# Performance work log

Hardware: AMD Instinct MI355X
Metric: run time of the kernel (lower is better)

The kernel has to match this reference:

```python
import jax, jax.numpy as jnp
import numpy as np

R_SPHERE = 3.0   # bounding_sphere_radius
NEAR = 0.0       # near_distance
FAR = 100.0      # far_distance
SECANT_STEPS = 4 # manifold_secant_steps
EPS = 1e-4
R0 = 1.0         # base radius of analytic manifold field


def setup_inputs() -> dict:
    key = jax.random.key(0)
    ks = jax.random.split(key, 6)
    B, R, L, H = 4, 8192, 4, 64
    rays_o = jax.random.normal(ks[0], (B, R, 3), dtype=jnp.float32) * 0.2  # origins inside sphere
    rd = jax.random.normal(ks[1], (B, R, 3), dtype=jnp.float32)
    rays_d = rd / jnp.linalg.norm(rd, axis=-1, keepdims=True)
    levels = jnp.linspace(0.5, -0.5, L, dtype=jnp.float32)  # manifold_levels parameter
    W1 = jax.random.normal(ks[2], (3, H), dtype=jnp.float32) * 0.3
    b1 = jnp.zeros((H,), dtype=jnp.float32)
    W2 = jax.random.normal(ks[3], (H, 1), dtype=jnp.float32) * 0.1
    b2 = jnp.zeros((1,), dtype=jnp.float32)
    rays_idx = jax.random.randint(ks[4], (B, R), 0, B, dtype=jnp.int64) if jax.config.jax_enable_x64 else jax.random.randint(ks[4], (B, R), 0, B, dtype=jnp.int32)
    mask_gt = jnp.ones((B, R), dtype=bool)
    return {"rays_o": rays_o, "rays_d": rays_d, "levels": levels, "W1": W1, "b1": b1,
            "W2": W2, "b2": b2, "mask_gt": mask_gt, "rays_idx": rays_idx, "num_samples": 64}


def _ray_march(rays_o, rays_d, levels, W1, b1, W2, b2, num_samples):
    B, Rn = rays_o.shape[:2]
    N = B * Rn
    L = levels.shape[0]
    o = rays_o.reshape(N, 3)
    d = rays_d.reshape(N, 3)

    def manifold_fn(x):
        # analytic stand-in for M(x_d, idx): scalar field + validity mask
        h = jnp.tanh(x @ W1 + b1)
        nrm = jnp.linalg.norm(x, axis=-1)
        s = (h @ W2)[..., 0] + b2[0] + (R0 - nrm)
        return s, nrm < R_SPHERE

    # ray-sphere intersection (unit-norm directions assumed, as in source)
    b = jnp.sum(o * d, axis=-1)
    c = jnp.sum(o * o, axis=-1) - R_SPHERE ** 2
    disc = b * b - c
    hit = disc > 0
    sq = jnp.sqrt(jnp.where(hit, disc, 1.0))
    d_near = jnp.maximum(-b - sq, NEAR)
    d_far = jnp.minimum(-b + sq, FAR)
    mask_bound = hit & (d_near < d_far)

    # stratified (uniform) depth samples, (N, S)
    t = jnp.linspace(0.0, 1.0, num_samples, dtype=rays_o.dtype)[None, :]
    ds = d_near[:, None] * (1 - t) + d_far[:, None] * t
    x_d = o[:, None, :] + d[:, None, :] * ds[..., None]  # (N, S, 3)
    scal, m_valid = manifold_fn(x_d)                      # (N, S)

    # --- find_closest_interval ---
    S = num_samples
    dep_f, dep_b = ds[:, :-1], ds[:, 1:]
    sc_f, sc_b = scal[:, :-1], scal[:, 1:]
    m_pair = m_valid[:, :-1] & m_valid[:, 1:]
    l3 = levels[None, :, None]                            # (1, L, 1)
    in_interval = (sc_f[:, None, :] >= l3) & (l3 >= sc_b[:, None, :]) & m_pair[:, None, :]
    rank = jnp.sign(l3 - sc_b[:, None, :]) * jnp.arange(S - 1, 0, -1, dtype=scal.dtype)
    ind_closest = jnp.argmax(rank, axis=2)                # (N, L)
    ind_lowest = jnp.broadcast_to(jnp.argmin(sc_b, axis=1)[:, None], (N, L))
    mask_surface = jnp.any(in_interval, axis=2)
    idx = jnp.where(mask_surface, ind_closest, ind_lowest)
    d_front = jnp.take_along_axis(dep_f, idx, axis=1)
    d_back = jnp.take_along_axis(dep_b, idx, axis=1)
    s_front = jnp.take_along_axis(sc_f, idx, axis=1)
    s_back = jnp.take_along_axis(sc_b, idx, axis=1)

    # --- find_exact_intersection ---
    lr = levels[None, :]                                  # (1, L)
    s_diff = s_front - s_back
    m_vdiff = jnp.abs(s_diff) > EPS
    mask_intersect = (s_front >= lr) & (lr >= s_back)
    mask_secant = mask_intersect & m_vdiff
    s_diff_safe = jnp.where(m_vdiff, s_diff, 1.0)
    d_secant = ((lr - s_back) * d_front + (s_front - lr) * d_back) / s_diff_safe
    d_init = jnp.where(mask_secant, d_secant, d_back)

    # secant refinement (fixed step count; masked full-array updates replace
    # torch's boolean-indexed subset updates with identical math on masked lanes)
    dfs, dbs, sfs, sbs, dcur = d_front, d_back, s_front, s_back, d_init
    for _ in range(SECANT_STEPS):
        x_mid = o[:, None, :] + dcur[..., None] * d[:, None, :]  # (N, L, 3)
        s_mid, mv = manifold_fn(x_mid)
        upf = (s_mid > lr) & mv
        upb = (s_mid < lr) & mv
        dfs = jnp.where(upf, dcur, dfs)
        sfs = jnp.where(upf, s_mid, sfs)
        dbs = jnp.where(upb, dcur, dbs)
        sbs = jnp.where(upb, s_mid, sbs)
        sd = sfs - sbs
        ok = jnp.abs(sd) > EPS
        dcur = jnp.where(ok, ((lr - sbs) * dfs + (sfs - lr) * dbs) / jnp.where(ok, sd, 1.0), dcur)
    d_intersect = jnp.where(mask_secant, dcur, d_init)

    # sort intersections by depth (use_presort=False branch)
    order = jnp.argsort(d_intersect, axis=1)
    d_intersect = jnp.take_along_axis(d_intersect, order, axis=1)
    mask_intersect = jnp.take_along_axis(mask_intersect, order, axis=1)

    dist = jnp.where(mask_bound[:, None], d_intersect, 0.0).reshape(B, Rn, L)
    mask = (mask_intersect & mask_bound[:, None]).reshape(B, Rn, L)
    return dist, mask


def reference(rays_o, rays_d, levels, W1, b1, W2, b2, mask_gt, rays_idx, num_samples):
    # mask_gt / rays_idx are unused in eval mode (use_gt_mask_when_training=False,
    # analytic manifold_fn ignores batch index), kept for signature fidelity.
    return _ray_march(rays_o, rays_d, levels, W1, b1, W2, b2, num_samples)
```

## Files before the change

kernel.cpp:

```cpp
#include <hip/hip_runtime.h>
#include <cstdint>

#define R_SPHEREf 3.0f
#define NEARf 0.0f
#define FARf 100.0f
#define SECANT_STEPS 4
#define EPSf 1e-4f
#define R0f 1.0f
#define Hh 64
#define Lc 4
#define Sn 64

#define C_HI 2.88539004325866699f
#define C_LO 3.8519227871e-08f

typedef unsigned long long u64;

__device__ __forceinline__ float fastdiv(float a, float b) {
    float rcp = __builtin_amdgcn_rcpf(b);
    rcp = __builtin_fmaf(rcp, __builtin_fmaf(-b, rcp, 1.0f), rcp);
    return a * rcp;
}

__global__ __launch_bounds__(256) void manifold_render_kernel(
    const float* __restrict__ rays_o, const float* __restrict__ rays_d,
    const float* __restrict__ levels, const float* __restrict__ W1,
    const float* __restrict__ b1, const float* __restrict__ W2,
    const float* __restrict__ b2, float* __restrict__ out, int N)
{
    __shared__ float4 abq[4][2][Hh];

    const int tid = threadIdx.x;
    const int wave = tid >> 6;
    const int lane = tid & 63;
    const int half = lane >> 5;
    const int sl5  = lane & 31;
    const int rbase = blockIdx.x * 8 + wave * 2;
    if (rbase >= N) return;
    const int r  = rbase + half;
    const int rr = (r < N) ? r : (N - 1);

    const float b2v = b2[0];
    float lvl[Lc];
#pragma unroll
    for (int j = 0; j < Lc; ++j) lvl[j] = levels[j];

    const float ox = rays_o[3 * rr], oy = rays_o[3 * rr + 1], oz = rays_o[3 * rr + 2];
    const float dx = rays_d[3 * rr], dy = rays_d[3 * rr + 1], dz = rays_d[3 * rr + 2];

    const float bq = ox * dx + oy * dy + oz * dz;
    const float cq = ox * ox + oy * oy + oz * oz - R_SPHEREf * R_SPHEREf;
    const float disc = bq * bq - cq;
    const bool hit = disc > 0.0f;
    const float sqv = __builtin_amdgcn_sqrtf(hit ? disc : 1.0f);
    const float d_near = fmaxf(-bq - sqv, NEARf);
    const float d_far  = fminf(-bq + sqv, FARf);
    const bool mask_bound = hit && (d_near < d_far);
    const float delta = (d_far - d_near) * (1.0f / 63.0f);

    const float w1x = W1[lane], w1y = W1[Hh + lane], w1z = W1[2 * Hh + lane];
    const float w2lane = W2[lane];
    const float zq = -2.0f * w2lane;
    const float zs = copysignf(fmaxf(fabsf(zq), 1e-30f), zq);
    const float rz = __builtin_amdgcn_rcpf(zs);
    {
        const float Ah = __builtin_fmaf(oz, w1z, __builtin_fmaf(oy, w1y,
                         __builtin_fmaf(ox, w1x, b1[lane])));
        const float Bh = __builtin_fmaf(dz, w1z, __builtin_fmaf(dy, w1y, dx * w1x));
        const float A2 = __builtin_fmaf(Ah, C_LO, Ah * C_HI);
        const float B2 = __builtin_fmaf(Bh, C_LO, Bh * C_HI);
        const float Gh = __builtin_amdgcn_exp2f(B2 * (8.0f * delta));
        abq[wave][half][lane] = make_float4(A2, B2, rz, Gh);
        const float oxo = __shfl_xor(ox, 32), oyo = __shfl_xor(oy, 32), ozo = __shfl_xor(oz, 32);
        const float dxo = __shfl_xor(dx, 32), dyo = __shfl_xor(dy, 32), dzo = __shfl_xor(dz, 32);
        const float dlo = __shfl_xor(delta, 32);
        const float Aho = __builtin_fmaf(ozo, w1z, __builtin_fmaf(oyo, w1y,
                          __builtin_fmaf(oxo, w1x, b1[lane])));
        const float Bho = __builtin_fmaf(dzo, w1z, __builtin_fmaf(dyo, w1y, dxo * w1x));
        const float A2o = __builtin_fmaf(Aho, C_LO, Aho * C_HI);
        const float B2o = __builtin_fmaf(Bho, C_LO, Bho * C_HI);
        const float Gho = __builtin_amdgcn_exp2f(B2o * (8.0f * dlo));
        abq[wave][half ^ 1][lane] = make_float4(A2o, B2o, rz, Gho);
    }

    float w2sum = w2lane;
#pragma unroll
    for (int m = 1; m < 64; m <<= 1) w2sum += __shfl_xor(w2sum, m);
    const float sbase = w2sum + b2v + R0f;

    const int hg2 = (lane >> 3) & 3;
    const int sl  = lane & 7;
    const float dsl = __builtin_fmaf((float)sl, delta, d_near);

    const float4* __restrict__ ab = &abq[wave][half][0];
    float v[16], G[16], K[16];
#pragma unroll
    for (int j = 0; j < 16; ++j) {
        const float4 q = ab[hg2 + 4 * j];
        const float y = __builtin_fmaf(dsl, q.y, q.x);
        const float e0 = __builtin_amdgcn_exp2f(y);
        v[j] = __builtin_fmaf(e0, q.z, q.z);
        G[j] = q.w;
        K[j] = __builtin_fmaf(-q.z, q.w, q.z);
    }

    float accA = 0.0f, accB = 0.0f;
#pragma unroll
    for (int it = 0; it < 8; ++it) {
        if (it > 0) {
#pragma unroll
            for (int j = 0; j < 16; ++j) v[j] = __builtin_fmaf(v[j], G[j], K[j]);
        }
        float part;
        {
            float tq[4];
#pragma unroll
            for (int qd = 0; qd < 4; ++qd) {
                const float a = v[4 * qd], b = v[4 * qd + 1];
                const float c = v[4 * qd + 2], d = v[4 * qd + 3];
                const float n01 = a + b, d01 = a * b;
                const float n23 = c + d, d23 = c * d;
                const float num = __builtin_fmaf(n23, d01, n01 * d23);
                const float den = d01 * d23;
                tq[qd] = num * __builtin_amdgcn_rcpf(den);
            }
            part = (tq[0] + tq[1]) + (tq[2] + tq[3]);
        }
        part += __shfl_xor(part, 8);
        part += __shfl_xor(part, 16);
        if (it == hg2)     accA = part;
        if (it == hg2 + 4) accB = part;
    }

    const float tA = (float)sl5 * (1.0f / 63.0f);
    const float dsvA = d_near * (1.0f - tA) + d_far * tA;
    const float tB = (float)(sl5 + 32) * (1.0f / 63.0f);
    const float dsvB = d_near * (1.0f - tB) + d_far * tB;
    const float xA0 = ox + dx * dsvA, xA1 = oy + dy * dsvA, xA2 = oz + dz * dsvA;
    const float xB0 = ox + dx * dsvB, xB1 = oy + dy * dsvB, xB2 = oz + dz * dsvB;
    const float nrmA = __builtin_amdgcn_sqrtf(xA0 * xA0 + xA1 * xA1 + xA2 * xA2);
    const float nrmB = __builtin_amdgcn_sqrtf(xB0 * xB0 + xB1 * xB1 + xB2 * xB2);
    const float scalA = (accA + sbase) - nrmA;
    const float scalB = (accB + sbase) - nrmB;
    const bool validA = nrmA < R_SPHEREf;
    const bool validB = nrmB < R_SPHEREf;

    const u64 LO32 = 0xFFFFFFFFull;
    const u64 mInt = 0x7FFFFFFFFFFFFFFFull;
#define ASSEMBLE(bA, bB) (half ? (((bA) >> 32) | ((bB) & ~LO32)) \
                               : (((bA) & LO32) | ((bB) << 32)))
    const u64 bVA = __ballot(validA), bVB = __ballot(validB);
    const u64 mV  = ASSEMBLE(bVA, bVB);
    const u64 mIB = mV & (mV >> 1) & mInt;

    float scbA = __shfl_down(scalA, 1);
    const float sB0 = __shfl(scalB, half << 5);
    if (sl5 == 31) scbA = sB0;
    const float scbB = __shfl_down(scalB, 1);
    const float keyA = scbA;
    const float keyB = (sl5 < 31) ? scbB : INFINITY;
    float mnv = fminf(keyA, keyB);
#pragma unroll
    for (int m = 1; m < 32; m <<= 1) mnv = fminf(mnv, __shfl_xor(mnv, m));
    const u64 eqA = __ballot(keyA == mnv), eqB = __ballot(keyB == mnv);
    const int ind_lowest = __builtin_ctzll(ASSEMBLE(eqA, eqB));

    bool mintb[Lc], msec[Lc];
    float dinit[Lc];
    float g_dfs = 0.f, g_dbs = 0.f, g_sfs = 0.f, g_sbs = 0.f, g_dcur = 0.f, g_lr = 0.f;
    const int gl = (lane >> 3) & 3;

#pragma unroll
    for (int lv = 0; lv < Lc; ++lv) {
        const float l = lvl[lv];
        const u64 bLA = __ballot(scalA < l),  bLB = __ballot(scalB < l);
        const u64 bEA = __ballot(scalA == l), bEB = __ballot(scalB == l);
        const u64 bL = ASSEMBLE(bLA, bLB);
        const u64 bE = ASSEMBLE(bEA, bEB);
        const u64 bP = (bL >> 1) & mInt;
        const u64 bZ = (bE >> 1) & mInt;
        const u64 bI = (~bL) & (bP | bZ) & mIB;
        const int ind_closest = bP ? __builtin_ctzll(bP)
                                   : (bZ ? __builtin_ctzll(bZ) : (Sn - 2));
        const int idx  = bI ? ind_closest : ind_lowest;
        const int idx1 = idx + 1;

        const int src0 = (half << 5) | (idx & 31);
        const float sfA = __shfl(scalA, src0), sfB = __shfl(scalB, src0);
        const float s_front = (idx < 32) ? sfA : sfB;
        const int src1 = (half << 5) | (idx1 & 31);
        const float sbA2 = __shfl(scalA, src1), sbB2 = __shfl(scalB, src1);
        const float s_back = (idx1 < 32) ? sbA2 : sbB2;

        const float tf = (float)idx  * (1.0f / 63.0f);
        const float d_front = d_near * (1.0f - tf) + d_far * tf;
        const float tb = (float)idx1 * (1.0f / 63.0f);
        const float d_back  = d_near * (1.0f - tb) + d_far * tb;

        const bool mi = (s_front >= l) && (l >= s_back);
        const float sd = s_front - s_back;
        const bool vd = fabsf(sd) > EPSf;
        const bool ms = mi && vd;
        const float d_sec = fastdiv((l - s_back) * d_front + (s_front - l) * d_back,
                                    vd ? sd : 1.0f);
        const float di = ms ? d_sec : d_back;

        mintb[lv] = mi; msec[lv] = ms; dinit[lv] = di;
        if (gl == lv) {
            g_dfs = d_front; g_dbs = d_back; g_sfs = s_front; g_sbs = s_back;
            g_dcur = di; g_lr = l;
        }
    }

    const int sub = lane & 7;
    const float4* __restrict__ ab2 = &abq[wave][half][0];
    float4 sq[8];
#pragma unroll
    for (int j = 0; j < 8; ++j) sq[j] = ab2[sub + 8 * j];

#pragma unroll
    for (int it = 0; it < SECANT_STEPS; ++it) {
        const float mx0 = ox + g_dcur * dx, mx1 = oy + g_dcur * dy, mx2 = oz + g_dcur * dz;
        const float mn = __builtin_amdgcn_sqrtf(mx0 * mx0 + mx1 * mx1 + mx2 * mx2);
        float vv[8];
#pragma unroll
        for (int j = 0; j < 8; ++j) {
            const float y = __builtin_fmaf(g_dcur, sq[j].y, sq[j].x);
            const float e = __builtin_amdgcn_exp2f(y);
            vv[j] = __builtin_fmaf(e, sq[j].z, sq[j].z);
        }
        float tp[4];
#pragma unroll
        for (int p = 0; p < 4; ++p) {
            const float n = vv[2 * p] + vv[2 * p + 1];
            const float d = vv[2 * p] * vv[2 * p + 1];
            tp[p] = n * __builtin_amdgcn_rcpf(d);
        }
        float part = (tp[0] + tp[1]) + (tp[2] + tp[3]);
        part += __shfl_xor(part, 1);
        part += __shfl_xor(part, 2);
        part += __shfl_xor(part, 4);
        const float s_mid = (part + sbase) - mn;
        const bool mv = mn < R_SPHEREf;
        const bool upf = (s_mid > g_lr) && mv;
        const bool upb = (s_mid < g_lr) && mv;
        if (upf) { g_dfs = g_dcur; g_sfs = s_mid; }
        if (upb) { g_dbs = g_dcur; g_sbs = s_mid; }
        const float sd2 = g_sfs - g_sbs;
        const bool ok = fabsf(sd2) > EPSf;
        if (ok) g_dcur = fastdiv((g_lr - g_sbs) * g_dfs + (g_sfs - g_lr) * g_dbs, sd2);
    }

    float v0g, v1g, v2g, v3g;
    {
        const int gb = half << 5;
        const float dc0 = __shfl(g_dcur, gb);
        const float dc1 = __shfl(g_dcur, gb + 8);
        const float dc2 = __shfl(g_dcur, gb + 16);
        const float dc3 = __shfl(g_dcur, gb + 24);
        v0g = msec[0] ? dc0 : dinit[0];
        v1g = msec[1] ? dc1 : dinit[1];
        v2g = msec[2] ? dc2 : dinit[2];
        v3g = msec[3] ? dc3 : dinit[3];
    }
    int m0 = mintb[0], m1 = mintb[1], m2 = mintb[2], m3 = mintb[3];
    int i0 = 0, i1 = 1, i2 = 2, i3 = 3;

#define CSWAP(va, ia, ma, vb, ib, mb)                                    \
    { bool sw = (vb < va) || (vb == va && ib < ia);                      \
      if (sw) { float tv = va; va = vb; vb = tv;                         \
                int ti = ia; ia = ib; ib = ti;                           \
                int tm = ma; ma = mb; mb = tm; } }
    CSWAP(v0g, i0, m0, v1g, i1, m1);
    CSWAP(v2g, i2, m2, v3g, i3, m3);
    CSWAP(v0g, i0, m0, v2g, i2, m2);
    CSWAP(v1g, i1, m1, v3g, i3, m3);
    CSWAP(v1g, i1, m1, v2g, i2, m2);
#undef CSWAP

    const long long NL = (long long)N * Lc;
    if (sl5 < 2 * Lc && r < N) {
        const int k = sl5 & 3;
        const float dvs = (k == 0) ? v0g : (k == 1) ? v1g : (k == 2) ? v2g : v3g;
        const int   mms = (k == 0) ? m0 : (k == 1) ? m1 : (k == 2) ? m2 : m3;
        const bool isd = sl5 < Lc;
        const float val = isd ? (mask_bound ? dvs : 0.0f)
                              : ((mms && mask_bound) ? 1.0f : 0.0f);
        const long long off = (long long)r * Lc + k + (isd ? 0LL : NL);
        out[off] = val;
    }
}

extern "C" void kernel_launch(void* const* d_in, const int* in_sizes, int n_in,
                              void* d_out, int out_size, void* d_ws, size_t ws_size,
                              hipStream_t stream) {
    const float* rays_o = (const float*)d_in[0];
    const float* rays_d = (const float*)d_in[1];
    const float* levels = (const float*)d_in[2];
    const float* W1 = (const float*)d_in[3];
    const float* b1 = (const float*)d_in[4];
    const float* W2 = (const float*)d_in[5];
    const float* b2 = (const float*)d_in[6];
    float* out = (float*)d_out;

    const int N = in_sizes[0] / 3;
    const int blocks = (N + 7) / 8;
    manifold_render_kernel<<<blocks, 256, 0, stream>>>(
        rays_o, rays_d, levels, W1, b1, W2, b2, out, N);
}
```

Before: 106.5 us.

## Repartition hidden-unit sum: 8 hidden groups of 4 samples, 16 passes

Changes the per-wave work split for the MLP sum over the 64 hidden units. Each lane now holds 8 hidden units (instead of 16) for 4 sample slots and steps 16 times with a geometric recurrence of stride 4*delta. An extra shuffle stage reduces across the 8 hidden groups. This cuts register pressure, and launch_bounds now requests 8 waves per EU for higher occupancy. The cost is more passes, more shuffles, and longer recurrence chains that may lose precision.

```diff
diff --git a/kernel.cpp b/kernel.cpp
--- a/kernel.cpp
+++ b/kernel.cpp
@@ -22,7 +22,7 @@
     return a * rcp;
 }
 
-__global__ __launch_bounds__(256) void manifold_render_kernel(
+__global__ __launch_bounds__(256, 8) void manifold_render_kernel(
     const float* __restrict__ rays_o, const float* __restrict__ rays_d,
     const float* __restrict__ levels, const float* __restrict__ W1,
     const float* __restrict__ b1, const float* __restrict__ W2,
@@ -69,7 +69,7 @@
         const float Bh = __builtin_fmaf(dz, w1z, __builtin_fmaf(dy, w1y, dx * w1x));
         const float A2 = __builtin_fmaf(Ah, C_LO, Ah * C_HI);
         const float B2 = __builtin_fmaf(Bh, C_LO, Bh * C_HI);
-        const float Gh = __builtin_amdgcn_exp2f(B2 * (8.0f * delta));
+        const float Gh = __builtin_amdgcn_exp2f(B2 * (4.0f * delta));
         abq[wave][half][lane] = make_float4(A2, B2, rz, Gh);
         const float oxo = __shfl_xor(ox, 32), oyo = __shfl_xor(oy, 32), ozo = __shfl_xor(oz, 32);
         const float dxo = __shfl_xor(dx, 32), dyo = __shfl_xor(dy, 32), dzo = __shfl_xor(dz, 32);
@@ -79,7 +79,7 @@
         const float Bho = __builtin_fmaf(dzo, w1z, __builtin_fmaf(dyo, w1y, dxo * w1x));
         const float A2o = __builtin_fmaf(Aho, C_LO, Aho * C_HI);
         const float B2o = __builtin_fmaf(Bho, C_LO, Bho * C_HI);
-        const float Gho = __builtin_amdgcn_exp2f(B2o * (8.0f * dlo));
+        const float Gho = __builtin_amdgcn_exp2f(B2o * (4.0f * dlo));
         abq[wave][half ^ 1][lane] = make_float4(A2o, B2o, rz, Gho);
     }
 
@@ -88,15 +88,15 @@
     for (int m = 1; m < 64; m <<= 1) w2sum += __shfl_xor(w2sum, m);
     const float sbase = w2sum + b2v + R0f;
 
-    const int hg2 = (lane >> 3) & 3;
-    const int sl  = lane & 7;
-    const float dsl = __builtin_fmaf((float)sl, delta, d_near);
+    const int hg3 = (lane >> 2) & 7;
+    const int sl2 = lane & 3;
+    const float dsl = __builtin_fmaf((float)sl2, delta, d_near);
 
     const float4* __restrict__ ab = &abq[wave][half][0];
-    float v[16], G[16], K[16];
-#pragma unroll
-    for (int j = 0; j < 16; ++j) {
-        const float4 q = ab[hg2 + 4 * j];
+    float v[8], G[8], K[8];
+#pragma unroll
+    for (int j = 0; j < 8; ++j) {
+        const float4 q = ab[hg3 + 8 * j];
         const float y = __builtin_fmaf(dsl, q.y, q.x);
         const float e0 = __builtin_amdgcn_exp2f(y);
         v[j] = __builtin_fmaf(e0, q.z, q.z);
@@ -106,30 +106,29 @@
 
     float accA = 0.0f, accB = 0.0f;
 #pragma unroll
-    for (int it = 0; it < 8; ++it) {
-        if (it > 0) {
-#pragma unroll
-            for (int j = 0; j < 16; ++j) v[j] = __builtin_fmaf(v[j], G[j], K[j]);
+    for (int p = 0; p < 16; ++p) {
+        if (p > 0) {
+#pragma unroll
+            for (int j = 0; j < 8; ++j) v[j] = __builtin_fmaf(v[j], G[j], K[j]);
         }
         float part;
         {
-            float tq[4];
-#pragma unroll
-            for (int qd = 0; qd < 4; ++qd) {
-                const float a = v[4 * qd], b = v[4 * qd + 1];
-                const float c = v[4 * qd + 2], d = v[4 * qd + 3];
-                const float n01 = a + b, d01 = a * b;
-                const float n23 = c + d, d23 = c * d;
-                const float num = __builtin_fmaf(n23, d01, n01 * d23);
-                const float den = d01 * d23;
-                tq[qd] = num * __builtin_amdgcn_rcpf(den);
-            }
-            part = (tq[0] + tq[1]) + (tq[2] + tq[3]);
-        }
+            const float n01 = v[0] + v[1], d01 = v[0] * v[1];
+            const float n23 = v[2] + v[3], d23 = v[2] * v[3];
+            const float numA = __builtin_fmaf(n23, d01, n01 * d23);
+            const float denA = d01 * d23;
+            const float n45 = v[4] + v[5], d45 = v[4] * v[5];
+            const float n67 = v[6] + v[7], d67 = v[6] * v[7];
+            const float numB = __builtin_fmaf(n67, d45, n45 * d67);
+            const float denB = d45 * d67;
+            part = numA * __builtin_amdgcn_rcpf(denA);
+            part = __builtin_fmaf(numB, __builtin_amdgcn_rcpf(denB), part);
+        }
+        part += __shfl_xor(part, 4);
         part += __shfl_xor(part, 8);
         part += __shfl_xor(part, 16);
-        if (it == hg2)     accA = part;
-        if (it == hg2 + 4) accB = part;
+        if (p < 8)  { if (p == hg3)     accA = part; }
+        else        { if (p == hg3 + 8) accB = part; }
     }
 
     const float tA = (float)sl5 * (1.0f / 63.0f);
```

Result: slower. 220.6 us (+107.2%).
